# Kernel tuning notes

Hardware: AMD Instinct MI355X
Metric: run time of the kernel (lower is better)

Reference implementation:

```python
import jax, jax.numpy as jnp
import numpy as np

EPS = 1e-5
NEG_SLOPE = 0.2

def _conv(x, w, b, stride, pad):
    y = jax.lax.conv_general_dilated(x, w, (stride, stride), ((pad, pad), (pad, pad)),
                                     dimension_numbers=('NCHW', 'OIHW', 'NCHW'))
    return y + b[None, :, None, None]

def _conv_transpose(x, w, b):
    # PyTorch ConvTranspose2d(k=3, s=2, p=1, output_padding=1): equivalent to a
    # lhs-dilated conv with padding (k-1-p, k-1-p+op) = (1, 2). w is stored in the
    # already-flipped OIHW layout (out_ch, in_ch, 3, 3).
    y = jax.lax.conv_general_dilated(x, w, (1, 1), ((1, 2), (1, 2)), lhs_dilation=(2, 2),
                                     dimension_numbers=('NCHW', 'OIHW', 'NCHW'))
    return y + b[None, :, None, None]

def _inorm(x):
    # InstanceNorm2d, affine=False, biased variance over (H, W)
    m = jnp.mean(x, axis=(2, 3), keepdims=True)
    v = jnp.mean((x - m) ** 2, axis=(2, 3), keepdims=True)
    return (x - m) * jax.lax.rsqrt(v + EPS)

def _lrelu(x):
    return jnp.where(x >= 0, x, NEG_SLOPE * x)

def _reflect_pad1(x):
    return jnp.pad(x, ((0, 0), (0, 0), (1, 1), (1, 1)), mode='reflect')


def setup_inputs() -> dict:
    key = jax.random.key(0)
    ks = jax.random.split(key, 12)
    B, H, W, S = 8, 256, 256, 19
    inp = jax.random.normal(ks[0], (B, 3, H, W), dtype=jnp.float32)
    # one-hot semantic map (float, 0/1) like the repo's segmaps
    labels = jax.random.randint(ks[1], (B, H, W), 0, S)
    segmap = jax.nn.one_hot(labels, S, axis=1, dtype=jnp.float32)

    def w(k, o, i):
        return jax.random.normal(k, (o, i, 3, 3), dtype=jnp.float32) * (1.0 / np.sqrt(i * 9))

    return {
        'input': inp, 'segmap': segmap,
        'w0': w(ks[2], 32, 3),    'b0': jnp.zeros((32,), jnp.float32),
        'w1': w(ks[3], 64, 32),   'b1': jnp.zeros((64,), jnp.float32),
        'w2': w(ks[4], 128, 64),  'b2': jnp.zeros((128,), jnp.float32),
        'wt': w(ks[5], 256, 128), 'bt': jnp.zeros((256,), jnp.float32),
        'w3': w(ks[6], 512, 256), 'b3': jnp.zeros((512,), jnp.float32),
    }


def reference(input, segmap, w0, b0, w1, b1, w2, b2, wt, bt, w3, b3):
    # CNN backbone
    x = _conv(_reflect_pad1(input), w0, b0, 1, 0)   # [B,32,256,256]
    x = _lrelu(_inorm(x))
    x = _conv(x, w1, b1, 2, 1)                       # [B,64,128,128]
    x = _lrelu(_inorm(x))
    x = _conv(x, w2, b2, 2, 1)                       # [B,128,64,64]
    x = _lrelu(_inorm(x))
    x = _conv_transpose(x, wt, bt)                   # [B,256,128,128]
    x = _lrelu(_inorm(x))
    codes = jnp.tanh(_conv(_reflect_pad1(x), w3, b3, 1, 0))  # [B,512,128,128]

    # nearest-neighbor downsample of segmap to codes' spatial size (PyTorch floor rule)
    B, C, Hc, Wc = codes.shape
    Hs, Ws = segmap.shape[2], segmap.shape[3]
    hi = (jnp.arange(Hc) * Hs) // Hc
    wi = (jnp.arange(Wc) * Ws) // Wc
    seg = segmap[:, :, hi[:, None], wi[None, :]]     # [B,S,Hc,Wc]

    # fused segment mean pooling (replaces nested masked_select loop)
    m = (seg != 0).astype(codes.dtype)
    sums = jnp.einsum('bchw,bshw->bsc', codes, m)    # [B,S,C]
    cnt = jnp.sum(m, axis=(2, 3))[..., None]          # [B,S,1]
    return jnp.where(cnt > 0, sums / jnp.maximum(cnt, 1.0), 0.0)
```

## Files before the change

kernel.cpp:

```cpp
#include <hip/hip_runtime.h>


#define B 8

typedef __attribute__((ext_vector_type(8))) short short8;
typedef __attribute__((ext_vector_type(4))) float f32x4;

static __device__ __forceinline__ unsigned short f2bf(float f) {
  union { float f; unsigned u; } v;
  v.f = f;
  unsigned r = v.u + 0x7fffu + ((v.u >> 16) & 1u);
  return (unsigned short)(r >> 16);
}
static __device__ __forceinline__ float bf2f(unsigned short h) {
  union { unsigned u; float f; } v;
  v.u = (unsigned)h << 16;
  return v.f;
}
static __device__ __forceinline__ float tanh_fast(float x) {
  float ax = fabsf(x);
  ax = fminf(ax, 20.f);
  const float e = __expf(-2.f * ax);
  const float t = (1.f - e) / (1.f + e);
  return __builtin_copysignf(t, x);
}

static __device__ __forceinline__ void gload_lds16(const unsigned short* g,
                                                   unsigned short* l) {
  __builtin_amdgcn_global_load_lds(
      (const __attribute__((address_space(1))) unsigned int*)(const void*)g,
      (__attribute__((address_space(3))) unsigned int*)(void*)l, 16, 0, 0);
}

__global__ __launch_bounds__(256) void conv0_kernel(
    const float* __restrict__ in, const float* __restrict__ w,
    const float* __restrict__ bias, unsigned short* __restrict__ Xp0) {
  __shared__ float sw[32 * 27 + 32];
  for (int i = threadIdx.x; i < 32 * 27; i += 256) sw[i] = w[i];
  if (threadIdx.x < 32) sw[32 * 27 + threadIdx.x] = bias[threadIdx.x];
  __syncthreads();
  const int b = blockIdx.y;
  const int p = blockIdx.x * 256 + threadIdx.x;
  const int y = p >> 8, x = p & 255;
  const float* inb = in + (size_t)b * 3 * 65536;
  float v[27];
#pragma unroll
  for (int c = 0; c < 3; ++c) {
#pragma unroll
    for (int ky = 0; ky < 3; ++ky) {
      int iy = y + ky - 1;
      iy = iy < 0 ? -iy : (iy > 255 ? 510 - iy : iy);
#pragma unroll
      for (int kx = 0; kx < 3; ++kx) {
        int ix = x + kx - 1;
        ix = ix < 0 ? -ix : (ix > 255 ? 510 - ix : ix);
        v[c * 9 + ky * 3 + kx] = inb[c * 65536 + iy * 256 + ix];
      }
    }
  }
  unsigned short* ob =
      Xp0 + ((size_t)b * 258 * 258 + (size_t)(y + 1) * 258 + (x + 1)) * 32;
#pragma unroll
  for (int q = 0; q < 4; ++q) {
    union { short8 v8; unsigned short u[8]; } pk;
#pragma unroll
    for (int j = 0; j < 8; ++j) {
      const int co = q * 8 + j;
      float a = sw[32 * 27 + co];
#pragma unroll
      for (int k = 0; k < 27; ++k) a = fmaf(v[k], sw[co * 27 + k], a);
      pk.u[j] = f2bf(a);
    }
    *(short8*)(ob + q * 8) = pk.v8;
  }
}

template <int C, int WLOG, int STR, int SH, int ITER>
__global__ __launch_bounds__(256) void stats_px_kernel(
    const unsigned short* __restrict__ X, float* __restrict__ ssum,
    float* __restrict__ ssq) {
  constexpr int G = C / 8;
  constexpr int R = 256 / G;
  const int b = blockIdx.y;
  const int t = threadIdx.x;
  const int rg = t / G;
  const int cg = (t % G) * 8;
  const int px0 = blockIdx.x * (R * ITER);
  const unsigned short* Xb = X + (size_t)b * STR * STR * C;
  float s[8], q[8];
#pragma unroll
  for (int j = 0; j < 8; ++j) { s[j] = 0.f; q[j] = 0.f; }
  for (int i = 0; i < ITER; ++i) {
    const int p = px0 + i * R + rg;
    const int yy = p >> WLOG, xx = p & ((1 << WLOG) - 1);
    union { short8 v8; unsigned short u[8]; } pk;
    pk.v8 = *(const short8*)(Xb + ((size_t)(yy + SH) * STR + (xx + SH)) * C + cg);
#pragma unroll
    for (int j = 0; j < 8; ++j) {
      const float v = bf2f(pk.u[j]);
      s[j] += v;
      q[j] += v * v;
    }
  }
  __shared__ float sm[2][R][C];
#pragma unroll
  for (int j = 0; j < 8; ++j) {
    sm[0][rg][cg + j] = s[j];
    sm[1][rg][cg + j] = q[j];
  }
  __syncthreads();
  if (t < C) {
    float ts = 0.f, tq = 0.f;
    for (int g2 = 0; g2 < R; ++g2) {
      ts += sm[0][g2][t];
      tq += sm[1][g2][t];
    }
    atomicAdd(&ssum[b * C + t], ts);
    atomicAdd(&ssq[b * C + t], tq);
  }
}

template <int C, int WLOG, int STR, int SH>
__global__ __launch_bounds__(256) void apply_px_kernel(
    unsigned short* __restrict__ X, const float* __restrict__ ssum,
    const float* __restrict__ ssq) {
  constexpr int G = C / 8;
  const int b = blockIdx.y;
  const int i = blockIdx.x * 256 + threadIdx.x;
  const int p = i / G;
  const int cg = (i % G) * 8;
  const int yy = p >> WLOG, xx = p & ((1 << WLOG) - 1);
  constexpr float inv = 1.f / (float)(1 << (2 * WLOG));
  float m[8], r[8];
#pragma unroll
  for (int j = 0; j < 8; ++j) {
    const float mm = ssum[b * C + cg + j] * inv;
    float var = ssq[b * C + cg + j] * inv - mm * mm;
    var = var < 0.f ? 0.f : var;
    m[j] = mm;
    r[j] = rsqrtf(var + 1e-5f);
  }
  unsigned short* pp =
      X + (size_t)b * STR * STR * C + ((size_t)(yy + SH) * STR + (xx + SH)) * C + cg;
  union { short8 v8; unsigned short u[8]; } pk;
  pk.v8 = *(const short8*)pp;
#pragma unroll
  for (int j = 0; j < 8; ++j) {
    float v = bf2f(pk.u[j]);
    v = (v - m[j]) * r[j];
    v = v >= 0.f ? v : 0.2f * v;
    pk.u[j] = f2bf(v);
  }
  *(short8*)pp = pk.v8;
}

__global__ __launch_bounds__(256) void zpad0_kernel(unsigned short* __restrict__ Xp0) {
  const int b = blockIdx.x;
  unsigned short* Xb = Xp0 + (size_t)b * 258 * 258 * 32;
  const short8 z = {0, 0, 0, 0, 0, 0, 0, 0};
  for (int i = threadIdx.x; i < 258 * 4; i += 256) {
    const int c = i >> 2, q = (i & 3) * 8;
    *(short8*)(Xb + ((size_t)0 * 258 + c) * 32 + q) = z;
    *(short8*)(Xb + ((size_t)c * 258 + 0) * 32 + q) = z;
  }
}

__global__ __launch_bounds__(256) void w1prep_kernel(const float* __restrict__ w1,
                                                     unsigned short* __restrict__ w1b) {
  const int i = blockIdx.x * 256 + threadIdx.x;
  if (i >= 9 * 64 * 32) return;
  const int e = i & 7, lane = (i >> 3) & 63, cot = (i >> 9) & 3, tap = i >> 11;
  const int co = cot * 16 + (lane & 15);
  const int ci = (lane >> 4) * 8 + e;
  w1b[i] = f2bf(w1[((size_t)co * 32 + ci) * 9 + tap]);
}

__global__ __launch_bounds__(256, 3) void conv1_mfma_kernel(
    const unsigned short* __restrict__ Xp0, const unsigned short* __restrict__ w1b,
    const float* __restrict__ b1, unsigned short* __restrict__ Xp1) {
  const int raw = blockIdx.x;
  const int swz = (raw & 7) * 128 + (raw >> 3);
  const int b = swz >> 7;
  const int oy = swz & 127;

  __shared__ unsigned short Asw1[3084 * 8];

  const int t = threadIdx.x;
  const int lane = t & 63;
  const int wave = t >> 6;
  const int wm = wave >> 1, wn = wave & 1;
  const int lg = lane >> 4, lr = lane & 15;
  const int wslot = wave * 64;

  const unsigned short* Xb = Xp0 + (size_t)b * 258 * 258 * 32;

#pragma unroll
  for (int k = 0; k < 13; ++k) {
    int s;
    bool act = true;
    if (k < 12) s = t + k * 256;
    else { s = 3072 + lane; act = (wave == 0 && lane < 12); }
    const int r = s / 1028, rm = s % 1028, c = rm >> 2, hs = rm & 3;
    const int h = hs ^ ((c >> 1) & 3);
    const unsigned short* gsrc = Xb + ((size_t)(2 * oy + r) * 258 + c) * 32 + h * 8;
    unsigned short* ldst = (k < 12) ? (Asw1 + (size_t)(k * 256 + wslot) * 8)
                                    : (Asw1 + (size_t)3072 * 8);
    if (act) gload_lds16(gsrc, ldst);
  }

  f32x4 acc[4][2];
#pragma unroll
  for (int mt = 0; mt < 4; ++mt)
#pragma unroll
    for (int nt = 0; nt < 2; ++nt) {
      f32x4 z = {0.f, 0.f, 0.f, 0.f};
      acc[mt][nt] = z;
    }
  __syncthreads();

  const unsigned short* w1l = w1b + (size_t)lane * 8;
#pragma unroll
  for (int tap = 0; tap < 9; ++tap) {
    const int ky = tap / 3, kx = tap % 3;
    short8 bf[2];
#pragma unroll
    for (int nt = 0; nt < 2; ++nt)
      bf[nt] = *(const short8*)(w1l + (size_t)(tap * 4 + wn * 2 + nt) * 512);
    short8 af[4];
#pragma unroll
    for (int mt = 0; mt < 4; ++mt) {
      const int c = 2 * (wm * 64 + mt * 16 + lr) + kx;
      const int hh = lg ^ ((c >> 1) & 3);
      af[mt] = *(const short8*)(Asw1 + (size_t)(ky * 1028 + c * 4 + hh) * 8);
    }
#pragma unroll
    for (int nt = 0; nt < 2; ++nt)
#pragma unroll
      for (int mt = 0; mt < 4; ++mt)
        acc[mt][nt] = __builtin_amdgcn_mfma_f32_16x16x32_bf16(
            af[mt], bf[nt], acc[mt][nt], 0, 0, 0);
  }

  float b1v[2];
#pragma unroll
  for (int nt = 0; nt < 2; ++nt) b1v[nt] = b1[wn * 32 + nt * 16 + lr];
  unsigned short* yb =
      Xp1 + ((size_t)b * 130 * 130 + (size_t)(oy + 1) * 130) * 64;
#pragma unroll
  for (int mt = 0; mt < 4; ++mt) {
#pragma unroll
    for (int r = 0; r < 4; ++r) {
      const int px_ = wm * 64 + mt * 16 + lg * 4 + r;
#pragma unroll
      for (int nt = 0; nt < 2; ++nt) {
        const int co = wn * 32 + nt * 16 + lr;
        yb[(size_t)(px_ + 1) * 64 + co] = f2bf(acc[mt][nt][r] + b1v[nt]);
      }
    }
  }
}

__global__ __launch_bounds__(256) void zpad1_kernel(unsigned short* __restrict__ Xp1) {
  const int b = blockIdx.x;
  unsigned short* Xb = Xp1 + (size_t)b * 130 * 130 * 64;
  const short8 z = {0, 0, 0, 0, 0, 0, 0, 0};
  for (int i = threadIdx.x; i < 130 * 8; i += 256) {
    const int c = i >> 3, q = (i & 7) * 8;
    *(short8*)(Xb + ((size_t)0 * 130 + c) * 64 + q) = z;
    *(short8*)(Xb + ((size_t)c * 130 + 0) * 64 + q) = z;
  }
}

__global__ __launch_bounds__(256) void w2prep_kernel(const float* __restrict__ w2,
                                                     unsigned short* __restrict__ w2b) {
  const int i = blockIdx.x * 256 + threadIdx.x;
  if (i >= 9 * 128 * 64) return;
  const int e = i & 7, lane = (i >> 3) & 63, cc = (i >> 9) & 1;
  const int cot = (i >> 10) & 7, tap = i >> 13;
  const int co = cot * 16 + (lane & 15);
  const int ci = cc * 32 + (lane >> 4) * 8 + e;
  w2b[i] = f2bf(w2[((size_t)co * 64 + ci) * 9 + tap]);
}

__global__ __launch_bounds__(256, 3) void conv2_mfma_kernel(
    const unsigned short* __restrict__ Xp1, const unsigned short* __restrict__ w2b,
    const float* __restrict__ b2, unsigned short* __restrict__ X2p) {
  const int raw = blockIdx.x;
  const int swz = (raw & 7) * 64 + (raw >> 3);
  const int b = swz >> 6;
  const int oy = swz & 63;

  __shared__ unsigned short Asw2[3096 * 8];

  const int t = threadIdx.x;
  const int lane = t & 63;
  const int wave = t >> 6;
  const int wm = wave >> 1, wn = wave & 1;
  const int lg = lane >> 4, lr = lane & 15;
  const int wslot = wave * 64;

  const unsigned short* Xb = Xp1 + (size_t)b * 130 * 130 * 64;

#pragma unroll
  for (int k = 0; k < 13; ++k) {
    int s;
    bool act = true;
    if (k < 12) s = t + k * 256;
    else { s = 3072 + lane; act = (wave == 0 && lane < 24); }
    const int r = s / 1032, rm = s % 1032, c = rm >> 3, hs = rm & 7;
    const int h = hs ^ ((c >> 1) & 7);
    const unsigned short* gsrc = Xb + ((size_t)(2 * oy + r) * 130 + c) * 64 + h * 8;
    unsigned short* ldst = (k < 12) ? (Asw2 + (size_t)(k * 256 + wslot) * 8)
                                    : (Asw2 + (size_t)3072 * 8);
    if (act) gload_lds16(gsrc, ldst);
  }

  f32x4 acc[2][4];
#pragma unroll
  for (int mt = 0; mt < 2; ++mt)
#pragma unroll
    for (int nt = 0; nt < 4; ++nt) {
      f32x4 z = {0.f, 0.f, 0.f, 0.f};
      acc[mt][nt] = z;
    }
  __syncthreads();

  const unsigned short* w2l = w2b + (size_t)lane * 8;
#pragma unroll
  for (int tap = 0; tap < 9; ++tap) {
    const int ky = tap / 3, kx = tap % 3;
#pragma unroll
    for (int cc = 0; cc < 2; ++cc) {
      short8 bf[4];
#pragma unroll
      for (int nt = 0; nt < 4; ++nt)
        bf[nt] = *(const short8*)(
            w2l + (size_t)((tap * 8 + wn * 4 + nt) * 2 + cc) * 512);
      short8 af[2];
#pragma unroll
      for (int mt = 0; mt < 2; ++mt) {
        const int c = 2 * (wm * 32 + mt * 16 + lr) + kx;
        const int hh = (cc * 4 + lg) ^ ((c >> 1) & 7);
        af[mt] = *(const short8*)(Asw2 + (size_t)(ky * 1032 + c * 8 + hh) * 8);
      }
#pragma unroll
      for (int nt = 0; nt < 4; ++nt)
#pragma unroll
        for (int mt = 0; mt < 2; ++mt)
          acc[mt][nt] = __builtin_amdgcn_mfma_f32_16x16x32_bf16(
              af[mt], bf[nt], acc[mt][nt], 0, 0, 0);
    }
  }

  float b2v[4];
#pragma unroll
  for (int nt = 0; nt < 4; ++nt) b2v[nt] = b2[wn * 64 + nt * 16 + lr];
  unsigned short* yb = X2p + ((size_t)b * 65 * 65 + (size_t)oy * 65) * 128;
#pragma unroll
  for (int mt = 0; mt < 2; ++mt) {
#pragma unroll
    for (int r = 0; r < 4; ++r) {
      const int px_ = wm * 32 + mt * 16 + lg * 4 + r;
#pragma unroll
      for (int nt = 0; nt < 4; ++nt) {
        const int co = wn * 64 + nt * 16 + lr;
        yb[(size_t)px_ * 128 + co] = f2bf(acc[mt][nt][r] + b2v[nt]);
      }
    }
  }
}

__global__ __launch_bounds__(256) void zpad_x2_kernel(unsigned short* __restrict__ X2p) {
  const int b = blockIdx.x;
  unsigned short* Xb = X2p + (size_t)b * 65 * 65 * 128;
  for (int i = threadIdx.x; i < 129 * 128; i += 256) {
    const int j = i >> 7, ci = i & 127;
    size_t off;
    if (j < 65) off = ((size_t)64 * 65 + j) * 128 + ci;
    else off = ((size_t)(j - 65) * 65 + 64) * 128 + ci;
    Xb[off] = 0;
  }
}

__global__ __launch_bounds__(256) void wtprep_kernel(const float* __restrict__ wt,
                                                     unsigned short* __restrict__ Wtb2) {
  const int i = blockIdx.x * 256 + threadIdx.x;
  if (i >= 9 * 256 * 128) return;
  const int e = i & 7, lane = (i >> 3) & 63, c4 = (i >> 9) & 3;
  const int cot = (i >> 11) & 15, tap = i >> 15;
  const int co = cot * 16 + (lane & 15);
  const int ci = c4 * 32 + (lane >> 4) * 8 + e;
  Wtb2[i] = f2bf(wt[((size_t)co * 128 + ci) * 9 + tap]);
}

__global__ __launch_bounds__(256, 3) void convt_mfma_kernel(
    const unsigned short* __restrict__ X2p, const unsigned short* __restrict__ Wtb2,
    const float* __restrict__ bt, unsigned short* __restrict__ Y,
    float* __restrict__ ssumY, float* __restrict__ ssqY) {
  const int raw = blockIdx.x;
  const int swz = (raw & 7) * 256 + (raw >> 3);
  const int b = swz >> 8;
  const int rem = swz & 255;
  const int cls = rem >> 6;
  const int sy = rem & 63;
  const int py = cls & 1, px = cls >> 1;

  const int kyA = py ? 0 : 1, kxA = px ? 0 : 1;
  int tk[4], tdy[4], tdx[4];
  int ntaps = 0;
  tk[ntaps] = kyA * 3 + kxA; tdy[ntaps] = 0; tdx[ntaps] = 0; ++ntaps;
  if (px) { tk[ntaps] = kyA * 3 + 2; tdy[ntaps] = 0; tdx[ntaps] = 1; ++ntaps; }
  if (py) { tk[ntaps] = 6 + kxA; tdy[ntaps] = 1; tdx[ntaps] = 0; ++ntaps; }
  if (py && px) { tk[ntaps] = 8; tdy[ntaps] = 1; tdx[ntaps] = 1; ++ntaps; }

  __shared__ unsigned short As2[2080 * 8];

  const int t = threadIdx.x;
  const int lane = t & 63;
  const int wn = t >> 6;
  const int lg = lane >> 4, lr = lane & 15;
  const int co_w = wn * 64;

  const unsigned short* Xb = X2p + (size_t)b * 65 * 65 * 128;

#pragma unroll
  for (int k = 0; k < 9; ++k) {
    int s;
    bool act = true;
    if (k < 8) s = k * 256 + t;
    else { s = 2048 + lane; act = (wn == 0 && lane < 32); }
    const int r = s >= 1040 ? 1 : 0;
    const int rm = s - r * 1040;
    const int c = rm >> 4, hs = rm & 15;
    const int g = hs ^ (c & 7);
    const unsigned short* gsrc = Xb + ((size_t)(sy + r) * 65 + c) * 128 + g * 8;
    unsigned short* ldst =
        As2 + (size_t)(k < 8 ? (k * 256 + wn * 64) : 2048) * 8;
    if (act) gload_lds16(gsrc, ldst);
  }

  f32x4 acc[4][4];
#pragma unroll
  for (int mt = 0; mt < 4; ++mt)
#pragma unroll
    for (int nt = 0; nt < 4; ++nt) {
      f32x4 z = {0.f, 0.f, 0.f, 0.f};
      acc[mt][nt] = z;
    }
  __syncthreads();

  const unsigned short* wlane = Wtb2 + (size_t)lane * 8;
  for (int c8 = 0; c8 < 4; ++c8) {
    for (int tp = 0; tp < ntaps; ++tp) {
      const int dy = tdy[tp], dx = tdx[tp];
      short8 af[4];
#pragma unroll
      for (int mt = 0; mt < 4; ++mt) {
        const int c = mt * 16 + lr + dx;
        const int hs = (c8 * 4 + lg) ^ (c & 7);
        af[mt] = *(const short8*)(As2 + (size_t)((dy * 65 + c) * 16 + hs) * 8);
      }
      const unsigned short* wt_ =
          wlane + (size_t)(((tk[tp] * 16 + wn * 4) * 4) + c8) * 512;
#pragma unroll
      for (int nt = 0; nt < 4; ++nt) {
        const short8 bf = *(const short8*)(wt_ + (size_t)nt * (4 * 512));
#pragma unroll
        for (int mt = 0; mt < 4; ++mt)
          acc[mt][nt] = __builtin_amdgcn_mfma_f32_16x16x32_bf16(
              af[mt], bf, acc[mt][nt], 0, 0, 0);
      }
    }
  }

  const int oy = 2 * sy + py;
  unsigned short* Yb = Y + ((size_t)b * 16384 + (size_t)oy * 128 + px) * 256;
  float bco[4], sS[4], sQ[4];
#pragma unroll
  for (int nt = 0; nt < 4; ++nt) {
    bco[nt] = bt[co_w + nt * 16 + lr];
    sS[nt] = 0.f;
    sQ[nt] = 0.f;
  }
#pragma unroll
  for (int mt = 0; mt < 4; ++mt) {
#pragma unroll
    for (int r = 0; r < 4; ++r) {
      const int sx = mt * 16 + lg * 4 + r;
      unsigned short* yp = Yb + (size_t)(2 * sx) * 256 + co_w + lr;
#pragma unroll
      for (int nt = 0; nt < 4; ++nt) {
        const float v = acc[mt][nt][r] + bco[nt];
        yp[nt * 16] = f2bf(v);
        sS[nt] += v;
        sQ[nt] += v * v;
      }
    }
  }
#pragma unroll
  for (int nt = 0; nt < 4; ++nt) {
    sS[nt] += __shfl_xor(sS[nt], 16);
    sS[nt] += __shfl_xor(sS[nt], 32);
    sQ[nt] += __shfl_xor(sQ[nt], 16);
    sQ[nt] += __shfl_xor(sQ[nt], 32);
  }
  if (lg == 0) {
#pragma unroll
    for (int nt = 0; nt < 4; ++nt) {
      atomicAdd(&ssumY[b * 256 + co_w + nt * 16 + lr], sS[nt]);
      atomicAdd(&ssqY[b * 256 + co_w + nt * 16 + lr], sQ[nt]);
    }
  }
}

__global__ __launch_bounds__(256) void inorm_apply_kernel(
    const unsigned short* __restrict__ Y, const float* __restrict__ ssum,
    const float* __restrict__ ssq, unsigned short* __restrict__ Xpad) {
  const int b = blockIdx.y, sl = blockIdx.x;
  const int t = threadIdx.x;
  const int rg = t >> 5;
  const int c0 = (t & 31) * 8;
  float m[8], r[8];
#pragma unroll
  for (int j = 0; j < 8; ++j) {
    const float mm = ssum[b * 256 + c0 + j] * (1.f / 16384.f);
    float var = ssq[b * 256 + c0 + j] * (1.f / 16384.f) - mm * mm;
    var = var < 0.f ? 0.f : var;
    m[j] = mm;
    r[j] = rsqrtf(var + 1e-5f);
  }
  const unsigned short* base = Y + ((size_t)b * 16384 + sl * 256) * 256;
  unsigned short* dstb = Xpad + (size_t)b * 130 * 130 * 256;
  for (int i = 0; i < 32; ++i) {
    const int row = sl * 256 + rg + i * 8;
    const int yy = row >> 7, xx = row & 127;
    union { short8 v; unsigned short u[8]; } pk;
    pk.v = *(const short8*)(base + (size_t)(rg + i * 8) * 256 + c0);
#pragma unroll
    for (int j = 0; j < 8; ++j) {
      float v = bf2f(pk.u[j]);
      v = (v - m[j]) * r[j];
      v = v >= 0.f ? v : 0.2f * v;
      pk.u[j] = f2bf(v);
    }
    *(short8*)(dstb + ((size_t)(yy + 1) * 130 + (xx + 1)) * 256 + c0) = pk.v;
  }
}

__global__ __launch_bounds__(256) void pad_rows_kernel(unsigned short* __restrict__ Xp) {
  const int b = blockIdx.x >> 1, side = blockIdx.x & 1;
  unsigned short* Xb = Xp + (size_t)b * 130 * 130 * 256;
  const int dr = side ? 129 : 0, sr = side ? 127 : 2;
  for (int i = threadIdx.x; i < 4096; i += 256) {
    const int c = 1 + (i >> 5), o = (i & 31) * 8;
    *(short8*)(Xb + ((size_t)dr * 130 + c) * 256 + o) =
        *(const short8*)(Xb + ((size_t)sr * 130 + c) * 256 + o);
  }
}
__global__ __launch_bounds__(256) void pad_cols_kernel(unsigned short* __restrict__ Xp) {
  const int b = blockIdx.x >> 1, side = blockIdx.x & 1;
  unsigned short* Xb = Xp + (size_t)b * 130 * 130 * 256;
  const int dc = side ? 129 : 0, sc = side ? 127 : 2;
  for (int i = threadIdx.x; i < 130 * 32; i += 256) {
    const int r = i >> 5, o = (i & 31) * 8;
    *(short8*)(Xb + ((size_t)r * 130 + dc) * 256 + o) =
        *(const short8*)(Xb + ((size_t)r * 130 + sc) * 256 + o);
  }
}

__global__ __launch_bounds__(256) void wprep_kernel(const float* __restrict__ w3,
                                                    unsigned short* __restrict__ Wb2) {
  const int i = blockIdx.x * 256 + threadIdx.x;
  if (i >= 9 * 512 * 256) return;
  const int e = i & 7, lane = (i >> 3) & 63, c8 = (i >> 9) & 7;
  const int cot = (i >> 12) & 31, tap = i >> 17;
  const int co = cot * 16 + (lane & 15);
  const int ci = c8 * 32 + (lane >> 4) * 8 + e;
  Wb2[i] = f2bf(w3[((size_t)co * 256 + ci) * 9 + tap]);
}

__global__ __launch_bounds__(256) void label_kernel(
    const float* __restrict__ segmap, int* __restrict__ labels,
    float* __restrict__ cnt) {
  const int b = blockIdx.y;
  const int p = blockIdx.x * 256 + threadIdx.x;
  const int i = p >> 7, j = p & 127;
  const float* sp = segmap + (size_t)b * 19 * 65536 + (2 * i) * 256 + 2 * j;
  int lab = 0;
#pragma unroll
  for (int s = 0; s < 19; ++s)
    if (sp[(size_t)s * 65536] != 0.f) lab = s;
  labels[b * 16384 + p] = lab;
  atomicAdd(&cnt[b * 19 + lab], 1.0f);
}

__global__ __launch_bounds__(256, 4) void conv3_mfma_pool_kernel(
    const unsigned short* __restrict__ Xpad, const unsigned short* __restrict__ Wb2,
    const float* __restrict__ bias, const int* __restrict__ labels,
    float* __restrict__ sums) {
  const int raw = blockIdx.x;
  const int swz = (raw & 7) * 1024 + (raw >> 3);
  const int b = swz >> 10;
  const int rem = swz & 1023;
  const int strip = rem >> 2;
  const int coq = rem & 3;
  const int y = strip >> 1;
  const int x0 = (strip & 1) * 64;

  constexpr int SLOTS = 800;
  __shared__ unsigned short Asw[2 * SLOTS * 8];
  float* lsum = (float*)Asw;

  const int t = threadIdx.x;
  const int lane = t & 63;
  const int wave = t >> 6;
  const int lg = lane >> 4, lr = lane & 15;
  const int co_w = coq * 128 + wave * 32;

  const unsigned short* Xb = Xpad + (size_t)b * 130 * 130 * 256;

  const unsigned short* sp[4];
  {
#pragma unroll
    for (int k = 0; k < 4; ++k) {
      int s;
      if (k < 3) s = t + k * 256;
      else s = (t < 24) ? (768 + t) : 768;
      const int r = s / 264, rm = s % 264, c = rm >> 2, hs = rm & 3;
      const int E = r * 66 + c;
      const int h = hs ^ ((E >> 1) & 3);
      sp[k] = Xb + ((size_t)(y + r) * 130 + x0 + c) * 256 + h * 8;
    }
  }

  f32x4 acc[4][2];
#pragma unroll
  for (int mt = 0; mt < 4; ++mt)
#pragma unroll
    for (int nt = 0; nt < 2; ++nt) {
      f32x4 z = {0.f, 0.f, 0.f, 0.f};
      acc[mt][nt] = z;
    }

  const unsigned short* wlane = Wb2 + (size_t)lane * 8;

  const int wslot = wave * 64;
#define STAGE(bufSel, off)                                                   \
  {                                                                          \
    unsigned short* base_ = Asw + (bufSel) * (SLOTS * 8);                    \
    gload_lds16(sp[0] + (off), base_ + (size_t)wslot * 8);                   \
    gload_lds16(sp[1] + (off), base_ + (size_t)(wslot + 256) * 8);           \
    gload_lds16(sp[2] + (off), base_ + (size_t)(wslot + 512) * 8);           \
    if (wave == 0 && lane < 24)                                              \
      gload_lds16(sp[3] + (off), base_ + (size_t)768 * 8);                   \
  }

  STAGE(0, 0)
  __syncthreads();

  for (int c8 = 0; c8 < 8; ++c8) {
    if (c8 < 7) STAGE((c8 + 1) & 1, (c8 + 1) * 32)
    const unsigned short* Ab = Asw + (c8 & 1) * (SLOTS * 8);
#pragma unroll
    for (int ky = 0; ky < 3; ++ky) {
#pragma unroll
      for (int kx = 0; kx < 3; ++kx) {
        const unsigned short* wt_ =
            wlane +
            (size_t)(((ky * 3 + kx) * 32 + coq * 8 + wave * 2) * 8 + c8) * 512;
        short8 bfv[2];
#pragma unroll
        for (int nt = 0; nt < 2; ++nt)
          bfv[nt] = *(const short8*)(wt_ + (size_t)nt * (8 * 512));
        short8 af[4];
#pragma unroll
        for (int mt = 0; mt < 4; ++mt) {
          const int E = ky * 66 + mt * 16 + lr + kx;
          const int hh = lg ^ ((E >> 1) & 3);
          af[mt] = *(const short8*)(Ab + (size_t)E * 32 + hh * 8);
        }
#pragma unroll
        for (int nt = 0; nt < 2; ++nt) {
#pragma unroll
          for (int mt = 0; mt < 4; ++mt)
            acc[mt][nt] = __builtin_amdgcn_mfma_f32_16x16x32_bf16(
                af[mt], bfv[nt], acc[mt][nt], 0, 0, 0);
        }
      }
    }
    __syncthreads();
  }
#undef STAGE

  for (int i = t; i < 19 * 128; i += 256) lsum[i] = 0.f;
  __syncthreads();

  const int* labp = labels + b * 16384 + y * 128 + x0;
  float bco[2];
#pragma unroll
  for (int nt = 0; nt < 2; ++nt) bco[nt] = bias[co_w + nt * 16 + lr];
#pragma unroll
  for (int mt = 0; mt < 4; ++mt) {
#pragma unroll
    for (int r = 0; r < 4; ++r) {
      const int lab = labp[mt * 16 + lg * 4 + r];
#pragma unroll
      for (int nt = 0; nt < 2; ++nt) {
        const float v = tanh_fast(acc[mt][nt][r] + bco[nt]);
        atomicAdd(&lsum[lab * 128 + wave * 32 + nt * 16 + lr], v);
      }
    }
  }
  __syncthreads();
  for (int i = t; i < 19 * 128; i += 256) {
    const float v = lsum[i];
    if (v != 0.f) {
      const int sI = i >> 7, c = i & 127;
      atomicAdd(&sums[((size_t)b * 19 + sI) * 512 + coq * 128 + c], v);
    }
  }
}

__global__ __launch_bounds__(256) void finalize_kernel(
    const float* __restrict__ sums, const float* __restrict__ cnt,
    float* __restrict__ out) {
  const int i = blockIdx.x * 256 + threadIdx.x;
  if (i >= B * 19 * 512) return;
  const int bs = i >> 9;
  const float c = cnt[bs];
  out[i] = c > 0.f ? sums[i] / fmaxf(c, 1.f) : 0.f;
}

extern "C" void kernel_launch(void* const* d_in, const int* in_sizes, int n_in,
                              void* d_out, int out_size, void* d_ws,
                              size_t ws_size, hipStream_t stream) {
  const float* input = (const float*)d_in[0];
  const float* segmap = (const float*)d_in[1];
  const float* w0 = (const float*)d_in[2];
  const float* b0 = (const float*)d_in[3];
  const float* w1 = (const float*)d_in[4];
  const float* b1 = (const float*)d_in[5];
  const float* w2 = (const float*)d_in[6];
  const float* b2 = (const float*)d_in[7];
  const float* wt = (const float*)d_in[8];
  const float* bt = (const float*)d_in[9];
  const float* w3 = (const float*)d_in[10];
  const float* b3 = (const float*)d_in[11];
  float* out = (float*)d_out;

  unsigned short* Xpad = (unsigned short*)d_ws;
  unsigned short* X2p = Xpad + 34611200;
  unsigned short* Y = X2p + 4326400;
  float* sums = (float*)(Y + 33554432);
  float* cnt = sums + 77824;
  float* ssum0 = cnt + 152;
  float* ssq0 = ssum0 + 256;
  float* ssum1 = ssq0 + 256;
  float* ssq1 = ssum1 + 512;
  float* ssum2 = ssq1 + 512;
  float* ssq2 = ssum2 + 1024;
  float* ssumY = ssq2 + 1024;
  float* ssqY = ssumY + 2048;
  int* labels = (int*)(ssqY + 2048);
  unsigned short* Wb2 = (unsigned short*)(labels + 131072);
  unsigned short* Wtb2 = Wb2 + 1179648;
  unsigned short* w1b = Wtb2 + 294912;
  unsigned short* w2b = w1b + 18432;
  unsigned short* Xp0 = Y;
  unsigned short* Xp1 = Y + 17040384;

  hipMemsetAsync(sums, 0, (77824 + 152 + 7680) * sizeof(float), stream);

  wprep_kernel<<<dim3((9 * 512 * 256 + 255) / 256), 256, 0, stream>>>(w3, Wb2);
  wtprep_kernel<<<dim3((9 * 256 * 128 + 255) / 256), 256, 0, stream>>>(wt, Wtb2);
  w1prep_kernel<<<dim3((9 * 64 * 32 + 255) / 256), 256, 0, stream>>>(w1, w1b);
  w2prep_kernel<<<dim3((9 * 128 * 64 + 255) / 256), 256, 0, stream>>>(w2, w2b);

  conv0_kernel<<<dim3(256, B), 256, 0, stream>>>(input, w0, b0, Xp0);
  zpad0_kernel<<<dim3(B), 256, 0, stream>>>(Xp0);
  stats_px_kernel<32, 8, 258, 1, 16><<<dim3(64, B), 256, 0, stream>>>(Xp0, ssum0, ssq0);
  apply_px_kernel<32, 8, 258, 1><<<dim3(1024, B), 256, 0, stream>>>(Xp0, ssum0, ssq0);

  conv1_mfma_kernel<<<dim3(1024), 256, 0, stream>>>(Xp0, w1b, b1, Xp1);
  zpad1_kernel<<<dim3(B), 256, 0, stream>>>(Xp1);
  stats_px_kernel<64, 7, 130, 1, 16><<<dim3(32, B), 256, 0, stream>>>(Xp1, ssum1, ssq1);
  apply_px_kernel<64, 7, 130, 1><<<dim3(512, B), 256, 0, stream>>>(Xp1, ssum1, ssq1);

  conv2_mfma_kernel<<<dim3(512), 256, 0, stream>>>(Xp1, w2b, b2, X2p);
  zpad_x2_kernel<<<dim3(B), 256, 0, stream>>>(X2p);
  stats_px_kernel<128, 6, 65, 0, 16><<<dim3(16, B), 256, 0, stream>>>(X2p, ssum2, ssq2);
  apply_px_kernel<128, 6, 65, 0><<<dim3(256, B), 256, 0, stream>>>(X2p, ssum2, ssq2);

  convt_mfma_kernel<<<dim3(2048), 256, 0, stream>>>(X2p, Wtb2, bt, Y, ssumY, ssqY);
  inorm_apply_kernel<<<dim3(64, B), 256, 0, stream>>>(Y, ssumY, ssqY, Xpad);
  pad_rows_kernel<<<dim3(2 * B), 256, 0, stream>>>(Xpad);
  pad_cols_kernel<<<dim3(2 * B), 256, 0, stream>>>(Xpad);
  label_kernel<<<dim3(64, B), 256, 0, stream>>>(segmap, labels, cnt);
  conv3_mfma_pool_kernel<<<dim3(8192), 256, 0, stream>>>(Xpad, Wb2, b3, labels, sums);
  finalize_kernel<<<dim3((B * 19 * 512 + 255) / 256), 256, 0, stream>>>(sums, cnt, out);
}
```

Baseline: 913.9 us.

## Stage conv3 input in two 128-channel halves with wider swizzle, reorder block mapping

The final conv+pool kernel now loads 128 input channels per stage instead of 32, so the K loop has two load/compute phases rather than eight double-buffered ones. The LDS layout uses a 16-way XOR swizzle over 16-byte slots. Block order is changed so consecutive blocks share an output-channel quarter instead of a spatial strip, and launch bounds drop from 4 to 3 blocks per CU to fit the larger LDS tile. The aim is fewer barriers and better weight locality, but the kernel loses load/compute overlap (each stage is loaded and then waited on) and runs at lower occupancy.

```diff
diff --git a/kernel.cpp b/kernel.cpp
--- a/kernel.cpp
+++ b/kernel.cpp
@@ -594,7 +594,7 @@
   atomicAdd(&cnt[b * 19 + lab], 1.0f);
 }
 
-__global__ __launch_bounds__(256, 4) void conv3_mfma_pool_kernel(
+__global__ __launch_bounds__(256, 3) void conv3_mfma_pool_kernel(
     const unsigned short* __restrict__ Xpad, const unsigned short* __restrict__ Wb2,
     const float* __restrict__ bias, const int* __restrict__ labels,
     float* __restrict__ sums) {
@@ -602,13 +602,12 @@
   const int swz = (raw & 7) * 1024 + (raw >> 3);
   const int b = swz >> 10;
   const int rem = swz & 1023;
-  const int strip = rem >> 2;
-  const int coq = rem & 3;
+  const int coq = rem >> 8;
+  const int strip = rem & 255;
   const int y = strip >> 1;
   const int x0 = (strip & 1) * 64;
 
-  constexpr int SLOTS = 800;
-  __shared__ unsigned short Asw[2 * SLOTS * 8];
+  __shared__ unsigned short Asw[3200 * 8];
   float* lsum = (float*)Asw;
 
   const int t = threadIdx.x;
@@ -616,20 +615,21 @@
   const int wave = t >> 6;
   const int lg = lane >> 4, lr = lane & 15;
   const int co_w = coq * 128 + wave * 32;
+  const int wslot = wave * 64;
 
   const unsigned short* Xb = Xpad + (size_t)b * 130 * 130 * 256;
 
-  const unsigned short* sp[4];
+  const unsigned short* sp[13];
   {
 #pragma unroll
-    for (int k = 0; k < 4; ++k) {
+    for (int k = 0; k < 13; ++k) {
       int s;
-      if (k < 3) s = t + k * 256;
-      else s = (t < 24) ? (768 + t) : 768;
-      const int r = s / 264, rm = s % 264, c = rm >> 2, hs = rm & 3;
-      const int E = r * 66 + c;
-      const int h = hs ^ ((E >> 1) & 3);
-      sp[k] = Xb + ((size_t)(y + r) * 130 + x0 + c) * 256 + h * 8;
+      if (k < 12) s = t + k * 256;
+      else s = (wave < 2) ? (3072 + wave * 64 + lane) : 3072;
+      const int E = s >> 4, hs = s & 15;
+      const int r = E / 66, c = E % 66;
+      const int g = hs ^ (E & 15);
+      sp[k] = Xb + ((size_t)(y + r) * 130 + x0 + c) * 256 + g * 8;
     }
   }
 
@@ -644,53 +644,58 @@
 
   const unsigned short* wlane = Wb2 + (size_t)lane * 8;
 
-  const int wslot = wave * 64;
-#define STAGE(bufSel, off)                                                   \
+#define STAGE(H)                                                             \
   {                                                                          \
-    unsigned short* base_ = Asw + (bufSel) * (SLOTS * 8);                    \
-    gload_lds16(sp[0] + (off), base_ + (size_t)wslot * 8);                   \
-    gload_lds16(sp[1] + (off), base_ + (size_t)(wslot + 256) * 8);           \
-    gload_lds16(sp[2] + (off), base_ + (size_t)(wslot + 512) * 8);           \
-    if (wave == 0 && lane < 24)                                              \
-      gload_lds16(sp[3] + (off), base_ + (size_t)768 * 8);                   \
-  }
-
-  STAGE(0, 0)
-  __syncthreads();
-
-  for (int c8 = 0; c8 < 8; ++c8) {
-    if (c8 < 7) STAGE((c8 + 1) & 1, (c8 + 1) * 32)
-    const unsigned short* Ab = Asw + (c8 & 1) * (SLOTS * 8);
-#pragma unroll
-    for (int ky = 0; ky < 3; ++ky) {
-#pragma unroll
-      for (int kx = 0; kx < 3; ++kx) {
-        const unsigned short* wt_ =
-            wlane +
-            (size_t)(((ky * 3 + kx) * 32 + coq * 8 + wave * 2) * 8 + c8) * 512;
-        short8 bfv[2];
-#pragma unroll
-        for (int nt = 0; nt < 2; ++nt)
-          bfv[nt] = *(const short8*)(wt_ + (size_t)nt * (8 * 512));
-        short8 af[4];
-#pragma unroll
-        for (int mt = 0; mt < 4; ++mt) {
-          const int E = ky * 66 + mt * 16 + lr + kx;
-          const int hh = lg ^ ((E >> 1) & 3);
-          af[mt] = *(const short8*)(Ab + (size_t)E * 32 + hh * 8);
-        }
-#pragma unroll
-        for (int nt = 0; nt < 2; ++nt) {
-#pragma unroll
-          for (int mt = 0; mt < 4; ++mt)
-            acc[mt][nt] = __builtin_amdgcn_mfma_f32_16x16x32_bf16(
-                af[mt], bfv[nt], acc[mt][nt], 0, 0, 0);
-        }
-      }
-    }
-    __syncthreads();
-  }
+    _Pragma("unroll")                                                        \
+    for (int k = 0; k < 12; ++k)                                             \
+      gload_lds16(sp[k] + (H) * 128, Asw + (size_t)(k * 256 + wslot) * 8);   \
+    if (wave == 0) gload_lds16(sp[12] + (H) * 128, Asw + (size_t)3072 * 8);  \
+    if (wave == 1 && lane < 32)                                              \
+      gload_lds16(sp[12] + (H) * 128, Asw + (size_t)3136 * 8);               \
+  }
+
+#define COMPUTE(H)                                                           \
+  {                                                                          \
+    _Pragma("unroll")                                                        \
+    for (int kk = 0; kk < 4; ++kk) {                                         \
+      _Pragma("unroll")                                                      \
+      for (int tap = 0; tap < 9; ++tap) {                                    \
+        const int ky_ = tap / 3, kx_ = tap % 3;                              \
+        const unsigned short* wt_ =                                          \
+            wlane +                                                          \
+            (size_t)((tap * 32 + coq * 8 + wave * 2) * 8 + ((H) * 4 + kk)) * \
+                512;                                                         \
+        short8 bfv[2];                                                       \
+        bfv[0] = *(const short8*)(wt_);                                      \
+        bfv[1] = *(const short8*)(wt_ + (size_t)(8 * 512));                  \
+        short8 af[4];                                                        \
+        _Pragma("unroll")                                                    \
+        for (int mt = 0; mt < 4; ++mt) {                                     \
+          const int E = ky_ * 66 + mt * 16 + lr + kx_;                       \
+          const int hh = (kk * 4 + lg) ^ (E & 15);                           \
+          af[mt] = *(const short8*)(Asw + (size_t)(E * 16 + hh) * 8);        \
+        }                                                                    \
+        _Pragma("unroll")                                                    \
+        for (int nt = 0; nt < 2; ++nt) {                                     \
+          _Pragma("unroll")                                                  \
+          for (int mt = 0; mt < 4; ++mt)                                     \
+            acc[mt][nt] = __builtin_amdgcn_mfma_f32_16x16x32_bf16(           \
+                af[mt], bfv[nt], acc[mt][nt], 0, 0, 0);                      \
+        }                                                                    \
+      }                                                                      \
+    }                                                                        \
+  }
+
+  STAGE(0)
+  __syncthreads();
+  COMPUTE(0)
+  __syncthreads();
+  STAGE(1)
+  __syncthreads();
+  COMPUTE(1)
+  __syncthreads();
 #undef STAGE
+#undef COMPUTE
 
   for (int i = t; i < 19 * 128; i += 256) lsum[i] = 0.f;
   __syncthreads();
```

Measured after the change: 1.069 ms. 1.17x slower.
